# Performance work log

Measured on AMD Instinct MI355X. Metric: run time of the kernel, lower is better.

Reference implementation:

```python
import jax, jax.numpy as jnp
import numpy as np

DIM = 256
HEADS = 4
WIN = 128
PAD = (WIN - 1) // 2  # 63
SHIFT = WIN // 2      # 64
RED = 16              # SE reduction


def _hann(w):
    # torch.hann_window(w, periodic=False)
    n = jnp.arange(w, dtype=jnp.float32)
    return 0.5 * (1.0 - jnp.cos(2.0 * jnp.pi * n / (w - 1)))


def _layernorm(x, g, b, eps=1e-5):
    mu = jnp.mean(x, axis=-1, keepdims=True)
    var = jnp.var(x, axis=-1, keepdims=True)
    return (x - mu) * jax.lax.rsqrt(var + eps) * g + b


def _attend_windows(x, ln_g, ln_b, in_proj_w, in_proj_b, out_w, out_b):
    B, T, C = x.shape
    w = WIN
    h = HEADS
    d = C // h
    L = T + 2 * PAD - w + 1  # number of stride-1 windows (= T-1 for even w)
    y = _layernorm(x, ln_g, ln_b)
    y_pad = jnp.pad(y, ((0, 0), (PAD, PAD), (0, 0)))
    idx = jnp.arange(L)[:, None] + jnp.arange(w)[None, :]  # (L, w)
    win = y_pad[:, idx, :]  # (B, L, w, C) -- the unfold blowup
    win = win * _hann(w)[None, None, :, None]
    # fused qkv projection (torch MHA in_proj)
    qkv = jnp.einsum('blwc,ec->blwe', win, in_proj_w) + in_proj_b  # (B,L,w,3C)
    q, k, v = jnp.split(qkv, 3, axis=-1)
    q = q.reshape(B, L, w, h, d)
    k = k.reshape(B, L, w, h, d)
    v = v.reshape(B, L, w, h, d)
    scale = 1.0 / jnp.sqrt(jnp.asarray(d, dtype=x.dtype))
    scores = jnp.einsum('blqhd,blkhd->blhqk', q, k) * scale
    attn = jax.nn.softmax(scores, axis=-1)
    o = jnp.einsum('blhqk,blkhd->blqhd', attn, v).reshape(B, L, w, C)
    o = jnp.einsum('blwc,ec->blwe', o, out_w) + out_b  # out_proj
    # fold: overlap-add back to length T (crop padding)
    idx_flat = idx.reshape(-1)  # (L*w,)
    acc = jnp.zeros((B, T + 2 * PAD, C), dtype=x.dtype)
    acc = acc.at[:, idx_flat, :].add(o.reshape(B, L * w, C))
    y_out = acc[:, PAD:PAD + T, :]
    counts = jnp.zeros((T + 2 * PAD,), dtype=x.dtype).at[idx_flat].add(1.0)
    counts = counts[PAD:PAD + T]
    return y_out / (counts[None, :, None] + 1e-6)


def setup_inputs() -> dict:
    key = jax.random.key(0)
    ks = jax.random.split(key, 9)
    C = DIM
    s = 0.02
    return {
        'x': jax.random.normal(ks[0], (1, 1024, C), dtype=jnp.float32),
        'ln_g': jnp.ones((C,), jnp.float32),
        'ln_b': jnp.zeros((C,), jnp.float32),
        'in_proj_w': jax.random.normal(ks[1], (3 * C, C), jnp.float32) * s,
        'in_proj_b': jnp.zeros((3 * C,), jnp.float32),
        'out_w': jax.random.normal(ks[2], (C, C), jnp.float32) * s,
        'out_b': jnp.zeros((C,), jnp.float32),
        'proj_w': jax.random.normal(ks[3], (C, C), jnp.float32) * s,
        'proj_b': jnp.zeros((C,), jnp.float32),
        'se_w1': jax.random.normal(ks[4], (C // RED, C), jnp.float32) * s,
        'se_w2': jax.random.normal(ks[5], (C, C // RED), jnp.float32) * s,
    }


def reference(x, ln_g, ln_b, in_proj_w, in_proj_b, out_w, out_b, proj_w, proj_b, se_w1, se_w2):
    # T > window_size branch (1024 > 128)
    y_main = _attend_windows(x, ln_g, ln_b, in_proj_w, in_proj_b, out_w, out_b)
    x_shift = jnp.roll(x, SHIFT, axis=1)
    y_shift = _attend_windows(x_shift, ln_g, ln_b, in_proj_w, in_proj_b, out_w, out_b)
    y_shift = jnp.roll(y_shift, -SHIFT, axis=1)
    y = 0.5 * (y_main + y_shift)
    y = jnp.einsum('btc,ec->bte', y, proj_w) + proj_b  # proj (dropout p=0 -> identity)
    # SE module: global average over T, bottleneck MLP, sigmoid gate
    s = jnp.mean(y, axis=1)  # (B, C)
    s = jax.nn.relu(s @ se_w1.T)
    s = jax.nn.sigmoid(s @ se_w2.T)
    y = y * s[:, None, :]
    return x + y
```

## Files before the change

### kernel.cpp

```cpp
#include <hip/hip_runtime.h>

#define TLEN 1024
#define CDIM 256
#define NHEAD 4
#define HD 64
#define WIN_ 128
#define PADL 63
#define LWIN 1023
#define TPAD 1150
#define SW 32

typedef __attribute__((ext_vector_type(8))) short bf16x8;
typedef __attribute__((ext_vector_type(4))) float f32x4;

__device__ __forceinline__ int prow(int v, int t) {
  if (v == 0) return t;
  if (t < PADL || t >= PADL + TLEN) return t;
  int s = t - PADL;
  s = (s + (TLEN - 64)) & (TLEN - 1);
  return PADL + s;
}

__device__ __forceinline__ float hannf(int j) {
  return 0.5f * (1.0f - __cosf(6.283185307179586f * (float)j / 127.0f));
}

__device__ __forceinline__ float countf(int t) {
  int lo = t - 127; if (lo < 0) lo = 0;
  int hi = t;       if (hi > LWIN - 1) hi = LWIN - 1;
  return (float)(hi - lo + 1);
}

__device__ __forceinline__ unsigned short bfr(float f) {
  unsigned int u = __float_as_uint(f);
  u += 0x7FFFu + ((u >> 16) & 1u);
  return (unsigned short)(u >> 16);
}
__device__ __forceinline__ unsigned int pk2t(float a, float b) {
  return __builtin_amdgcn_perm(__float_as_uint(b), __float_as_uint(a), 0x07060302u);
}
__device__ __forceinline__ float bfu(unsigned short u) {
  return __uint_as_float(((unsigned int)u) << 16);
}
__device__ __forceinline__ float bflo(unsigned int u) { return __uint_as_float(u << 16); }
__device__ __forceinline__ float bfhi(unsigned int u) { return __uint_as_float(u & 0xFFFF0000u); }

__global__ void k_prep(const float* __restrict__ x, const float* __restrict__ g,
                       const float* __restrict__ b, unsigned short* __restrict__ lnbf,
                       const float* __restrict__ W, unsigned short* __restrict__ Wb,
                       const float* __restrict__ pw, const float* __restrict__ ow,
                       const float* __restrict__ ob, unsigned short* __restrict__ Mtb,
                       float* __restrict__ vbv,
                       float* __restrict__ accg, unsigned short* __restrict__ Pbf,
                       float* __restrict__ msum) {
  __shared__ float pr[256];
  __shared__ float red[256];
  const int bid = blockIdx.x;
  const int tid = threadIdx.x;
  if (bid < 256) {
    int wv = tid >> 6, lane = tid & 63;
    int r = bid * 4 + wv;
    float4 v = ((const float4*)(x + (size_t)r * CDIM))[lane];
    float s = v.x + v.y + v.z + v.w;
    float q = v.x * v.x + v.y * v.y + v.z * v.z + v.w * v.w;
    #pragma unroll
    for (int m = 32; m >= 1; m >>= 1) { s += __shfl_xor(s, m); q += __shfl_xor(q, m); }
    float mu = s * (1.0f / 256.0f);
    float var = q * (1.0f / 256.0f) - mu * mu;
    float rs = rsqrtf(var + 1e-5f);
    float4 gg = ((const float4*)g)[lane];
    float4 bb = ((const float4*)b)[lane];
    uint2 o;
    o.x = (unsigned int)bfr((v.x - mu) * rs * gg.x + bb.x) |
          ((unsigned int)bfr((v.y - mu) * rs * gg.y + bb.y) << 16);
    o.y = (unsigned int)bfr((v.z - mu) * rs * gg.z + bb.z) |
          ((unsigned int)bfr((v.w - mu) * rs * gg.w + bb.w) << 16);
    ((uint2*)(lnbf + (size_t)r * CDIM))[lane] = o;
  } else if (bid < 352) {
    int i = (bid - 256) * 256 + tid;
    const float4* src = (const float4*)W;
    float4 a = src[2 * i], c = src[2 * i + 1];
    uint4 o;
    o.x = (unsigned int)bfr(a.x) | ((unsigned int)bfr(a.y) << 16);
    o.y = (unsigned int)bfr(a.z) | ((unsigned int)bfr(a.w) << 16);
    o.z = (unsigned int)bfr(c.x) | ((unsigned int)bfr(c.y) << 16);
    o.w = (unsigned int)bfr(c.z) | ((unsigned int)bfr(c.w) << 16);
    ((uint4*)Wb)[i] = o;
  } else if (bid < 608) {
    const int e = bid - 352;
    pr[tid] = pw[(size_t)e * CDIM + tid];
    __syncthreads();
    float a0 = 0.f, a1 = 0.f, a2 = 0.f, a3 = 0.f;
    for (int m = 0; m < 256; m += 4) {
      a0 += pr[m] * ow[(size_t)m * CDIM + tid];
      a1 += pr[m + 1] * ow[(size_t)(m + 1) * CDIM + tid];
      a2 += pr[m + 2] * ow[(size_t)(m + 2) * CDIM + tid];
      a3 += pr[m + 3] * ow[(size_t)(m + 3) * CDIM + tid];
    }
    Mtb[(size_t)e * CDIM + tid] = bfr((a0 + a1) + (a2 + a3));
    red[tid] = pr[tid] * ob[tid];
    __syncthreads();
    for (int s = 128; s > 0; s >>= 1) { if (tid < s) red[tid] += red[tid + s]; __syncthreads(); }
    if (tid == 0) vbv[e] = red[0];
  } else if (bid < 624) {
    uint4 zz = make_uint4(0, 0, 0, 0);
    for (int i = (bid - 608) * 256 + tid; i < 147200; i += 16 * 256)
      ((uint4*)accg)[i] = zz;
  } else {
    uint4 zz = make_uint4(0, 0, 0, 0);
    for (int i = (bid - 624) * 256 + tid; i < 12096; i += 16 * 256) {
      int idx = (i < 6048) ? i : (104352 + (i - 6048));
      ((uint4*)Pbf)[idx] = zz;
    }
    if (bid == 624 && tid < 64) ((float4*)msum)[tid] = make_float4(0.f, 0.f, 0.f, 0.f);
  }
}

__launch_bounds__(512, 1)
__global__ void k_proj(const unsigned short* __restrict__ lnbf,
                       const unsigned short* __restrict__ Wb,
                       unsigned short* __restrict__ Pbf) {
  __shared__ __align__(16) unsigned short Ps[64 * 128];
  const int tid = threadIdx.x;
  const int lane = tid & 63, wv = tid >> 6;
  const int li16 = lane & 15, q4 = lane >> 4;
  const int ws = wv & 1, we = wv >> 1;
  const int sbase = blockIdx.x * 64;
  const int ebase = blockIdx.y * 128;
  const int s0 = sbase + ws * 32;
  const int e0 = ebase + we * 32;

  f32x4 acc[2][2];
  #pragma unroll
  for (int it = 0; it < 2; ++it)
    #pragma unroll
    for (int et = 0; et < 2; ++et) acc[it][et] = (f32x4){0.f, 0.f, 0.f, 0.f};

  #pragma unroll
  for (int ks = 0; ks < 8; ++ks) {
    bf16x8 Af[2], Bf[2];
    #pragma unroll
    for (int it = 0; it < 2; ++it)
      Af[it] = *(const bf16x8*)(lnbf + (size_t)(s0 + 16 * it + li16) * 256 + ks * 32 + q4 * 8);
    #pragma unroll
    for (int et = 0; et < 2; ++et)
      Bf[et] = *(const bf16x8*)(Wb + (size_t)(e0 + 16 * et + li16) * 256 + ks * 32 + q4 * 8);
    #pragma unroll
    for (int it = 0; it < 2; ++it)
      #pragma unroll
      for (int et = 0; et < 2; ++et)
        acc[it][et] = __builtin_amdgcn_mfma_f32_16x16x32_bf16(Af[it], Bf[et], acc[it][et], 0, 0, 0);
  }
  #pragma unroll
  for (int it = 0; it < 2; ++it)
    #pragma unroll
    for (int et = 0; et < 2; ++et)
      #pragma unroll
      for (int r = 0; r < 4; ++r) {
        int lr = ws * 32 + 16 * it + 4 * q4 + r;
        int lc = we * 32 + 16 * et + li16;
        Ps[lr * 128 + lc] = bfr(acc[it][et][r]);
      }
  __syncthreads();
  for (int i = tid; i < 1024; i += 512) {
    int r = i >> 4, c = (i & 15) * 8;
    *(uint4*)(Pbf + (size_t)(PADL + sbase + r) * 768 + ebase + c) = *(uint4*)&Ps[r * 128 + c];
  }
}

__device__ __forceinline__ void stage_v(const unsigned short* __restrict__ Pbf,
                                        unsigned short* vt, int v, int hd,
                                        int l0, int w, int tid,
                                        const float* __restrict__ bB,
                                        const float* __restrict__ hth) {
  const int jp = tid & 63;
  const int dg = tid >> 6;
  const int j0 = 2 * jp;
  const int p0 = w + j0;
  int row0 = prow(v, l0 + w + j0);
  int row1 = prow(v, l0 + w + j0 + 1);
  uint4 a = *(const uint4*)(Pbf + (size_t)row0 * 768 + 512 + hd * 64 + dg * 8);
  uint4 b = *(const uint4*)(Pbf + (size_t)row1 * 768 + 512 + hd * 64 + dg * 8);
  float h0 = hth[j0], h1 = hth[j0 + 1];
  float e0 = __expf(h0 * bB[p0] * 0.125f);
  float e1 = __expf(h1 * bB[p0 + 1] * 0.125f);
  float f0 = e0 * h0, f1 = e1 * h1;
  unsigned int av[4] = {a.x, a.y, a.z, a.w};
  unsigned int bv[4] = {b.x, b.y, b.z, b.w};
  #pragma unroll
  for (int q = 0; q < 4; ++q) {
    int d0 = dg * 8 + 2 * q;
    unsigned int w0 = pk2t(f0 * bflo(av[q]), f1 * bflo(bv[q]));
    unsigned int w1 = pk2t(f0 * bfhi(av[q]), f1 * bfhi(bv[q]));
    *(unsigned int*)&vt[d0 * 128 + (j0 ^ ((d0 & 7) << 3))] = w0;
    *(unsigned int*)&vt[(d0 + 1) * 128 + (j0 ^ (((d0 + 1) & 7) << 3))] = w1;
  }
  if (tid < 64) {
    *(unsigned int*)&vt[64 * 128 + j0] = pk2t(e0, e1);
  }
}

__launch_bounds__(512, 2)
__global__ void k_attn(const unsigned short* __restrict__ Pbf, const float* __restrict__ ipb,
                       float* __restrict__ accg) {
  __shared__ __align__(16) unsigned short Pq[159 * 64];
  __shared__ __align__(16) unsigned short Pk[159 * 64];
  __shared__ __align__(16) unsigned short Vt[2][80 * 128];
  __shared__ __align__(16) unsigned short Ab[128 * 128];
  __shared__ __align__(16) float accs[159 * 68];
  __shared__ float hth[128];
  __shared__ float bB[160];
  __shared__ float bqS[64];

  const int strip = blockIdx.x, hd = blockIdx.y, v = blockIdx.z;
  const int l0 = strip * SW;
  const int nw = (SW < LWIN - l0) ? SW : (LWIN - l0);
  const int span = nw - 1 + WIN_;
  const int tid = threadIdx.x;
  const int lane = tid & 63, wv = tid >> 6;
  const int li16 = lane & 15, q4 = lane >> 4;
  const int iw = 16 * wv + li16;

  for (int i = tid; i < 159 * 68; i += 512) accs[i] = 0.0f;
  if (tid < 128) hth[tid] = hannf(tid);
  if (tid < 64) bqS[tid] = ipb[hd * 64 + tid];
  for (int i = tid; i < span * 8; i += 512) {
    int t = i >> 3, dg = i & 7;
    int row = prow(v, l0 + t);
    const unsigned short* src = Pbf + (size_t)row * 768 + hd * 64;
    uint4 q = *(const uint4*)(src + dg * 8);
    uint4 k = *(const uint4*)(src + 256 + dg * 8);
    int off = (dg * 8) ^ ((t & 7) << 3);
    *(uint4*)&Pq[t * 64 + off] = q;
    *(uint4*)&Pk[t * 64 + off] = k;
  }
  {
    uint4 zz = make_uint4(0, 0, 0, 0);
    for (int i = tid; i < 480; i += 512) {
      int bidx = i / 240, k = i % 240;
      *(uint4*)&Vt[bidx][65 * 128 + k * 8] = zz;
    }
  }
  __syncthreads();

  for (int p = tid; p < span; p += 512) {
    float b = 0.0f;
    int sw = (p & 7) << 3;
    for (int d = 0; d < 64; ++d) b += bqS[d] * bfu(Pk[p * 64 + (d ^ sw)]);
    bB[p] = b;
  }
  __syncthreads();
  stage_v(Pbf, &Vt[0][0], v, hd, l0, 0, tid, bB, hth);
  __syncthreads();

  float hh[32];
  {
    const float h_i = hth[iw];
    #pragma unroll
    for (int tj = 0; tj < 8; ++tj)
      #pragma unroll
      for (int r = 0; r < 4; ++r)
        hh[tj * 4 + r] = h_i * hth[16 * tj + 4 * q4 + r] * 0.125f;
  }

  #pragma unroll 1
  for (int w = 0; w < nw; ++w) {
    bf16x8 Qf[2];
    {
      int t = w + iw, sw = (t & 7) << 3;
      Qf[0] = *(bf16x8*)&Pq[t * 64 + ((8 * q4) ^ sw)];
      Qf[1] = *(bf16x8*)&Pq[t * 64 + ((32 + 8 * q4) ^ sw)];
    }
    f32x4 S[8];
    #pragma unroll
    for (int tj = 0; tj < 8; ++tj) S[tj] = (f32x4){0.f, 0.f, 0.f, 0.f};
    #pragma unroll
    for (int tj = 0; tj < 8; ++tj) {
      int t = w + 16 * tj + li16, sw = (t & 7) << 3;
      bf16x8 Kf0 = *(bf16x8*)&Pk[t * 64 + ((8 * q4) ^ sw)];
      bf16x8 Kf1 = *(bf16x8*)&Pk[t * 64 + ((32 + 8 * q4) ^ sw)];
      S[tj] = __builtin_amdgcn_mfma_f32_16x16x32_bf16(Kf0, Qf[0], S[tj], 0, 0, 0);
      S[tj] = __builtin_amdgcn_mfma_f32_16x16x32_bf16(Kf1, Qf[1], S[tj], 0, 0, 0);
    }

    #pragma unroll
    for (int tj = 0; tj < 8; ++tj)
      #pragma unroll
      for (int r = 0; r < 4; ++r)
        S[tj][r] = __expf(hh[tj * 4 + r] * S[tj][r]);

    {
      int sw = (iw & 7) << 3;
      #pragma unroll
      for (int tj = 0; tj < 8; ++tj) {
        uint2 o;
        o.x = pk2t(S[tj][0], S[tj][1]);
        o.y = pk2t(S[tj][2], S[tj][3]);
        *(uint2*)&Ab[iw * 128 + ((16 * tj + 4 * q4) ^ sw)] = o;
      }
    }

    f32x4 O[5];
    #pragma unroll
    for (int mt = 0; mt < 5; ++mt) O[mt] = (f32x4){0.f, 0.f, 0.f, 0.f};
    const unsigned short* vt = &Vt[w & 1][0];
    {
      int swi = (iw & 7) << 3;
      #pragma unroll
      for (int ks = 0; ks < 4; ++ks) {
        bf16x8 Bf = *(bf16x8*)&Ab[iw * 128 + ((32 * ks + 8 * q4) ^ swi)];
        #pragma unroll
        for (int mt = 0; mt < 5; ++mt) {
          int d = 16 * mt + li16;
          bf16x8 Af = *(bf16x8*)&vt[d * 128 + ((32 * ks + 8 * q4) ^ ((d & 7) << 3))];
          O[mt] = __builtin_amdgcn_mfma_f32_16x16x32_bf16(Af, Bf, O[mt], 0, 0, 0);
        }
      }
    }

    float nn = __shfl(O[4][0], li16);
    float sc = 1.0f / nn;

    {
      float* arow = &accs[(w + iw) * 68];
      #pragma unroll
      for (int mt = 0; mt < 4; ++mt) {
        int c = 16 * mt + 4 * q4;
        float4 cur = *(float4*)&arow[c];
        cur.x += O[mt][0] * sc; cur.y += O[mt][1] * sc;
        cur.z += O[mt][2] * sc; cur.w += O[mt][3] * sc;
        *(float4*)&arow[c] = cur;
      }
    }

    if (w + 1 < nw) stage_v(Pbf, &Vt[(w + 1) & 1][0], v, hd, l0, w + 1, tid, bB, hth);
    __syncthreads();
  }

  float* av = accg + (size_t)v * TPAD * CDIM;
  for (int i = tid; i < span * 64; i += 512) {
    int p = i >> 6, dd = i & 63;
    int lo = p - 127; if (lo < 0) lo = 0;
    int hi = p; if (hi > nw - 1) hi = nw - 1;
    float cnt = (float)(hi - lo + 1);
    float bvd = ipb[512 + hd * 64 + dd];
    atomicAdd(&av[(size_t)(l0 + p) * CDIM + hd * 64 + dd],
              accs[p * 68 + dd] + cnt * bvd);
  }
}

__launch_bounds__(512, 2)
__global__ void k_comb(const float* __restrict__ accg, const unsigned short* __restrict__ Mtb,
                       const float* __restrict__ vbv, const float* __restrict__ pb,
                       float* __restrict__ z, float* __restrict__ msum) {
  __shared__ __align__(16) unsigned short Ub[32 * 264];
  __shared__ float cfA[32], cfB[32], bscL[32];
  __shared__ float msB[128];
  const int tid = threadIdx.x;
  const int lane = tid & 63, wv = tid >> 6;
  const int li16 = lane & 15, q4 = lane >> 4;
  const int t0 = blockIdx.x * 32;
  const int e0 = blockIdx.y * 128;

  if (tid < 32) {
    int s = t0 + tid;
    float c0 = countf(PADL + s);
    float c1 = countf(PADL + ((s + 64) & (TLEN - 1)));
    float fA = 0.5f / (c0 + 1e-6f), fB = 0.5f / (c1 + 1e-6f);
    cfA[tid] = fA; cfB[tid] = fB;
    bscL[tid] = c0 * fA + c1 * fB;
  }
  if (tid < 128) msB[tid] = 0.0f;
  __syncthreads();

  for (int i = tid; i < 32 * 128; i += 512) {
    int rr = i >> 7, c2 = (i & 127) * 2;
    int s = t0 + rr;
    int s1 = (s + 64) & (TLEN - 1);
    float2 a0 = *(const float2*)&accg[(size_t)(PADL + s) * CDIM + c2];
    float2 a1 = *(const float2*)&accg[(size_t)TPAD * CDIM + (size_t)(PADL + s1) * CDIM + c2];
    float fA = cfA[rr], fB = cfB[rr];
    *(unsigned int*)&Ub[rr * 264 + c2] =
        pk2t(a0.x * fA + a1.x * fB, a0.y * fA + a1.y * fB);
  }
  __syncthreads();

  f32x4 acc[2];
  acc[0] = (f32x4){0.f, 0.f, 0.f, 0.f};
  acc[1] = (f32x4){0.f, 0.f, 0.f, 0.f};
  #pragma unroll
  for (int ks = 0; ks < 8; ++ks) {
    bf16x8 Bf = *(const bf16x8*)(Mtb + (size_t)(e0 + wv * 16 + li16) * 256 + ks * 32 + q4 * 8);
    #pragma unroll
    for (int it = 0; it < 2; ++it) {
      bf16x8 Af = *(bf16x8*)&Ub[(16 * it + li16) * 264 + ks * 32 + q4 * 8];
      acc[it] = __builtin_amdgcn_mfma_f32_16x16x32_bf16(Af, Bf, acc[it], 0, 0, 0);
    }
  }

  {
    int e = e0 + wv * 16 + li16;
    float vbe = vbv[e], pbe = pb[e];
    float part = 0.0f;
    #pragma unroll
    for (int it = 0; it < 2; ++it)
      #pragma unroll
      for (int r = 0; r < 4; ++r) {
        int rloc = 16 * it + 4 * q4 + r;
        float val = acc[it][r] + bscL[rloc] * vbe + pbe;
        z[(size_t)(t0 + rloc) * CDIM + e] = val;
        part += val;
      }
    atomicAdd(&msB[e - e0], part);
  }
  __syncthreads();
  if (tid < 128) atomicAdd(&msum[e0 + tid], msB[tid]);
}

__global__ void k_finalse(const float* __restrict__ x, const float* __restrict__ z,
                          const float* __restrict__ msum, const float* __restrict__ w1,
                          const float* __restrict__ w2, float* __restrict__ out) {
  __shared__ float red2[16][4];
  __shared__ float s1[16];
  __shared__ float gateS[256];
  int tid = threadIdx.x;
  int lane = tid & 63, wv = tid >> 6;
  float sm = msum[tid] * (1.0f / 1024.0f);
  #pragma unroll
  for (int r = 0; r < 16; ++r) {
    float v = sm * w1[(size_t)r * 256 + tid];
    #pragma unroll
    for (int m = 32; m >= 1; m >>= 1) v += __shfl_xor(v, m);
    if (lane == 0) red2[r][wv] = v;
  }
  __syncthreads();
  if (tid < 16) {
    float a = red2[tid][0] + red2[tid][1] + red2[tid][2] + red2[tid][3];
    s1[tid] = fmaxf(a, 0.0f);
  }
  __syncthreads();
  float gacc = 0.0f;
  #pragma unroll
  for (int i = 0; i < 16; ++i) gacc += s1[i] * w2[(size_t)tid * 16 + i];
  gateS[tid] = 1.0f / (1.0f + __expf(-gacc));
  __syncthreads();
  int i = blockIdx.x * 256 + tid;
  float4 xv = ((const float4*)x)[i];
  float4 zv = ((const float4*)z)[i];
  float4 gv = ((const float4*)gateS)[i & 63];
  float4 o;
  o.x = xv.x + zv.x * gv.x;
  o.y = xv.y + zv.y * gv.y;
  o.z = xv.z + zv.z * gv.z;
  o.w = xv.w + zv.w * gv.w;
  ((float4*)out)[i] = o;
}

extern "C" void kernel_launch(void* const* d_in, const int* in_sizes, int n_in,
                              void* d_out, int out_size, void* d_ws, size_t ws_size,
                              hipStream_t stream) {
  const float* x   = (const float*)d_in[0];
  const float* lng = (const float*)d_in[1];
  const float* lnb = (const float*)d_in[2];
  const float* ipw = (const float*)d_in[3];
  const float* ipb = (const float*)d_in[4];
  const float* ow  = (const float*)d_in[5];
  const float* ob  = (const float*)d_in[6];
  const float* pw  = (const float*)d_in[7];
  const float* pb  = (const float*)d_in[8];
  const float* w1  = (const float*)d_in[9];
  const float* w2  = (const float*)d_in[10];
  float* out = (float*)d_out;

  float* ws = (float*)d_ws;
  unsigned short* lnbf = (unsigned short*)ws;
  unsigned short* Wb   = (unsigned short*)(ws + 131072);
  unsigned short* Pbf  = (unsigned short*)(ws + 229376);
  float* accg = ws + 229376 + 441600;
  unsigned short* Mtb = (unsigned short*)(accg + 588800);
  float* vbv  = accg + 588800 + 32768;
  float* z    = vbv + 256;
  float* msum = z + 262144;

  k_prep<<<dim3(640), dim3(256), 0, stream>>>(x, lng, lnb, lnbf, ipw, Wb,
                                              pw, ow, ob, Mtb, vbv, accg, Pbf, msum);
  k_proj<<<dim3(16, 6), dim3(512), 0, stream>>>(lnbf, Wb, Pbf);
  k_attn<<<dim3(32, NHEAD, 2), dim3(512), 0, stream>>>(Pbf, ipb, accg);
  k_comb<<<dim3(32, 2), dim3(512), 0, stream>>>(accg, Mtb, vbv, pb, z, msum);
  k_finalse<<<dim3(256), dim3(256), 0, stream>>>(x, z, msum, w1, w2, out);
}
```

Baseline: 192.5 us.

## Precompute banded QK scores once per strip instead of per window

Overlapping windows share most of their query-key dot products, differing only by the per-window Hann weights, which are applied separately. The kernel now computes the whole 160x160 band of raw Q·K products once per strip with MFMA, stores it in LDS as bf16, and each window reads its slice with 16-bit realignment before applying hann weights and exp. This removes the per-window QK MFMAs and the Ab LDS round trip. Pq/Pk share LDS with the accumulator buffer to fit the band, at the cost of an extra bf16 rounding of the scores and unaligned band reads.

```diff
diff --git a/kernel.cpp b/kernel.cpp
--- a/kernel.cpp
+++ b/kernel.cpp
@@ -44,6 +44,8 @@
 }
 __device__ __forceinline__ float bflo(unsigned int u) { return __uint_as_float(u << 16); }
 __device__ __forceinline__ float bfhi(unsigned int u) { return __uint_as_float(u & 0xFFFF0000u); }
+
+#define AL16(h, l) ((((unsigned int)(l)) >> 16) | (((unsigned int)(h)) << 16))
 
 __global__ void k_prep(const float* __restrict__ x, const float* __restrict__ g,
                        const float* __restrict__ b, unsigned short* __restrict__ lnbf,
@@ -203,14 +205,16 @@
 __launch_bounds__(512, 2)
 __global__ void k_attn(const unsigned short* __restrict__ Pbf, const float* __restrict__ ipb,
                        float* __restrict__ accg) {
-  __shared__ __align__(16) unsigned short Pq[159 * 64];
-  __shared__ __align__(16) unsigned short Pk[159 * 64];
+  __shared__ __align__(16) unsigned short band[160 * 168];
   __shared__ __align__(16) unsigned short Vt[2][80 * 128];
-  __shared__ __align__(16) unsigned short Ab[128 * 128];
-  __shared__ __align__(16) float accs[159 * 68];
+  __shared__ __align__(16) unsigned char uni[159 * 68 * 4];
   __shared__ float hth[128];
   __shared__ float bB[160];
   __shared__ float bqS[64];
+
+  unsigned short* Pq = (unsigned short*)uni;
+  unsigned short* Pk = Pq + 159 * 64;
+  float* accs = (float*)uni;
 
   const int strip = blockIdx.x, hd = blockIdx.y, v = blockIdx.z;
   const int l0 = strip * SW;
@@ -221,7 +225,6 @@
   const int li16 = lane & 15, q4 = lane >> 4;
   const int iw = 16 * wv + li16;
 
-  for (int i = tid; i < 159 * 68; i += 512) accs[i] = 0.0f;
   if (tid < 128) hth[tid] = hannf(tid);
   if (tid < 64) bqS[tid] = ipb[hd * 64 + tid];
   for (int i = tid; i < span * 8; i += 512) {
@@ -249,72 +252,84 @@
     for (int d = 0; d < 64; ++d) b += bqS[d] * bfu(Pk[p * 64 + (d ^ sw)]);
     bB[p] = b;
   }
-  __syncthreads();
+  for (int tile = wv; tile < 100; tile += 8) {
+    int ta = tile / 10, tb = tile - 10 * (tile / 10);
+    int tqa = 16 * ta + li16, swq = (tqa & 7) << 3;
+    bf16x8 Aq0 = *(bf16x8*)&Pq[tqa * 64 + ((8 * q4) ^ swq)];
+    bf16x8 Aq1 = *(bf16x8*)&Pq[tqa * 64 + ((32 + 8 * q4) ^ swq)];
+    int tkb = 16 * tb + li16, swk = (tkb & 7) << 3;
+    bf16x8 Bk0 = *(bf16x8*)&Pk[tkb * 64 + ((8 * q4) ^ swk)];
+    bf16x8 Bk1 = *(bf16x8*)&Pk[tkb * 64 + ((32 + 8 * q4) ^ swk)];
+    f32x4 D = (f32x4){0.f, 0.f, 0.f, 0.f};
+    D = __builtin_amdgcn_mfma_f32_16x16x32_bf16(Aq0, Bk0, D, 0, 0, 0);
+    D = __builtin_amdgcn_mfma_f32_16x16x32_bf16(Aq1, Bk1, D, 0, 0, 0);
+    #pragma unroll
+    for (int r = 0; r < 4; ++r)
+      band[(16 * ta + 4 * q4 + r) * 168 + 16 * tb + li16] = bfr(D[r]);
+  }
+  __syncthreads();
+
+  for (int i = tid; i < 159 * 68; i += 512) accs[i] = 0.0f;
   stage_v(Pbf, &Vt[0][0], v, hd, l0, 0, tid, bB, hth);
   __syncthreads();
 
-  float hh[32];
+  float hh2[32];
   {
     const float h_i = hth[iw];
     #pragma unroll
-    for (int tj = 0; tj < 8; ++tj)
+    for (int ks = 0; ks < 4; ++ks)
       #pragma unroll
-      for (int r = 0; r < 4; ++r)
-        hh[tj * 4 + r] = h_i * hth[16 * tj + 4 * q4 + r] * 0.125f;
+      for (int jj = 0; jj < 8; ++jj)
+        hh2[ks * 8 + jj] = h_i * hth[32 * ks + 8 * q4 + jj] * 0.125f;
   }
 
   #pragma unroll 1
   for (int w = 0; w < nw; ++w) {
-    bf16x8 Qf[2];
-    {
-      int t = w + iw, sw = (t & 7) << 3;
-      Qf[0] = *(bf16x8*)&Pq[t * 64 + ((8 * q4) ^ sw)];
-      Qf[1] = *(bf16x8*)&Pq[t * 64 + ((32 + 8 * q4) ^ sw)];
-    }
-    f32x4 S[8];
-    #pragma unroll
-    for (int tj = 0; tj < 8; ++tj) S[tj] = (f32x4){0.f, 0.f, 0.f, 0.f};
-    #pragma unroll
-    for (int tj = 0; tj < 8; ++tj) {
-      int t = w + 16 * tj + li16, sw = (t & 7) << 3;
-      bf16x8 Kf0 = *(bf16x8*)&Pk[t * 64 + ((8 * q4) ^ sw)];
-      bf16x8 Kf1 = *(bf16x8*)&Pk[t * 64 + ((32 + 8 * q4) ^ sw)];
-      S[tj] = __builtin_amdgcn_mfma_f32_16x16x32_bf16(Kf0, Qf[0], S[tj], 0, 0, 0);
-      S[tj] = __builtin_amdgcn_mfma_f32_16x16x32_bf16(Kf1, Qf[1], S[tj], 0, 0, 0);
-    }
-
-    #pragma unroll
-    for (int tj = 0; tj < 8; ++tj)
+    const int m = w & 7;
+    const unsigned short* brow = &band[(w + iw) * 168 + (w & ~7)];
+    const unsigned short* vt = &Vt[w & 1][0];
+
+    f32x4 O[5];
+    #pragma unroll
+    for (int mt = 0; mt < 5; ++mt) O[mt] = (f32x4){0.f, 0.f, 0.f, 0.f};
+
+    #pragma unroll
+    for (int ks = 0; ks < 4; ++ks) {
+      uint4 R0 = *(const uint4*)&brow[32 * ks + 8 * q4];
+      uint4 R1 = *(const uint4*)&brow[32 * ks + 8 * q4 + 8];
+      unsigned int d0 = R0.x, d1 = R0.y, d2 = R0.z, d3 = R0.w;
+      unsigned int d4 = R1.x, d5 = R1.y, d6 = R1.z, d7 = R1.w;
+      unsigned int o0, o1, o2, o3;
+      switch (m) {
+        case 0: o0 = d0; o1 = d1; o2 = d2; o3 = d3; break;
+        case 1: o0 = AL16(d1, d0); o1 = AL16(d2, d1); o2 = AL16(d3, d2); o3 = AL16(d4, d3); break;
+        case 2: o0 = d1; o1 = d2; o2 = d3; o3 = d4; break;
+        case 3: o0 = AL16(d2, d1); o1 = AL16(d3, d2); o2 = AL16(d4, d3); o3 = AL16(d5, d4); break;
+        case 4: o0 = d2; o1 = d3; o2 = d4; o3 = d5; break;
+        case 5: o0 = AL16(d3, d2); o1 = AL16(d4, d3); o2 = AL16(d5, d4); o3 = AL16(d6, d5); break;
+        case 6: o0 = d3; o1 = d4; o2 = d5; o3 = d6; break;
+        default: o0 = AL16(d4, d3); o1 = AL16(d5, d4); o2 = AL16(d6, d5); o3 = AL16(d7, d6); break;
+      }
+      float a0 = __expf(hh2[ks * 8 + 0] * bflo(o0));
+      float a1 = __expf(hh2[ks * 8 + 1] * bfhi(o0));
+      float a2 = __expf(hh2[ks * 8 + 2] * bflo(o1));
+      float a3 = __expf(hh2[ks * 8 + 3] * bfhi(o1));
+      float a4 = __expf(hh2[ks * 8 + 4] * bflo(o2));
+      float a5 = __expf(hh2[ks * 8 + 5] * bfhi(o2));
+      float a6 = __expf(hh2[ks * 8 + 6] * bflo(o3));
+      float a7 = __expf(hh2[ks * 8 + 7] * bfhi(o3));
+      union { uint4 u; bf16x8 f; } cvt;
+      cvt.u.x = pk2t(a0, a1);
+      cvt.u.y = pk2t(a2, a3);
+      cvt.u.z = pk2t(a4, a5);
+      cvt.u.w = pk2t(a6, a7);
+      bf16x8 Bf = cvt.f;
+
       #pragma unroll
-      for (int r = 0; r < 4; ++r)
-        S[tj][r] = __expf(hh[tj * 4 + r] * S[tj][r]);
-
-    {
-      int sw = (iw & 7) << 3;
-      #pragma unroll
-      for (int tj = 0; tj < 8; ++tj) {
-        uint2 o;
-        o.x = pk2t(S[tj][0], S[tj][1]);
-        o.y = pk2t(S[tj][2], S[tj][3]);
-        *(uint2*)&Ab[iw * 128 + ((16 * tj + 4 * q4) ^ sw)] = o;
-      }
-    }
-
-    f32x4 O[5];
-    #pragma unroll
-    for (int mt = 0; mt < 5; ++mt) O[mt] = (f32x4){0.f, 0.f, 0.f, 0.f};
-    const unsigned short* vt = &Vt[w & 1][0];
-    {
-      int swi = (iw & 7) << 3;
-      #pragma unroll
-      for (int ks = 0; ks < 4; ++ks) {
-        bf16x8 Bf = *(bf16x8*)&Ab[iw * 128 + ((32 * ks + 8 * q4) ^ swi)];
-        #pragma unroll
-        for (int mt = 0; mt < 5; ++mt) {
-          int d = 16 * mt + li16;
-          bf16x8 Af = *(bf16x8*)&vt[d * 128 + ((32 * ks + 8 * q4) ^ ((d & 7) << 3))];
-          O[mt] = __builtin_amdgcn_mfma_f32_16x16x32_bf16(Af, Bf, O[mt], 0, 0, 0);
-        }
+      for (int mt = 0; mt < 5; ++mt) {
+        int d = 16 * mt + li16;
+        bf16x8 Af = *(bf16x8*)&vt[d * 128 + ((32 * ks + 8 * q4) ^ ((d & 7) << 3))];
+        O[mt] = __builtin_amdgcn_mfma_f32_16x16x32_bf16(Af, Bf, O[mt], 0, 0, 0);
       }
     }
 
```

New measurement: 186.3 us. 3.2% less time.
